# Optimization experiments

Hardware: AMD Instinct MI355X
Metric: run time of the kernel (lower is better)

Reference implementation:

```python
import jax, jax.numpy as jnp
import numpy as np

G, M_PER_GROUP, K, N = 8, 2048, 4096, 4096  # experts, tokens/expert, d_model, expert out dim


def setup_inputs() -> dict:
    key = jax.random.key(0)
    k1, k2, k3, k4 = jax.random.split(key, 4)
    T = G * M_PER_GROUP
    # int8 quantized activations [total_tokens, K] and per-expert weights [G, N, K] ('NT' layout)
    i8_left_tensor = jax.random.randint(k1, (T, K), -127, 128, dtype=jnp.int32).astype(jnp.int8)
    i8_right_tensors = jax.random.randint(k2, (G, N, K), -127, 128, dtype=jnp.int32).astype(jnp.int8)
    # per-token and per-(group, out-channel) dequant scales
    left_scales = jax.random.uniform(k3, (T,), jnp.float32, 0.001, 0.02)
    right_scales = jax.random.uniform(k4, (G, N), jnp.float32, 0.001, 0.02)
    tokens_per_group = jnp.full((G,), M_PER_GROUP, dtype=jnp.int32)
    return {
        "i8_left_tensor": i8_left_tensor,
        "i8_right_tensors": i8_right_tensors,
        "left_scales": left_scales,
        "right_scales": right_scales,
        "tokens_per_group": tokens_per_group,
    }


def reference(i8_left_tensor, i8_right_tensors, left_scales, right_scales, tokens_per_group):
    # moe_w8a8_group_gemm, 'NT': per group g, out_g = (A_g @ B_g^T) * ls_g[:, None] * rs_g[None, :] -> fp16
    g, n, k = i8_right_tensors.shape
    t = i8_left_tensor.shape[0]
    m = t // g  # equal-sized groups (tokens_per_group is constant M_PER_GROUP)
    a = i8_left_tensor.reshape(g, m, k).astype(jnp.float32)   # [G, M, K]
    b = i8_right_tensors.astype(jnp.float32)                  # [G, N, K]
    acc = jnp.einsum('gmk,gnk->gmn', a, b)                    # int8xint8 accum in f32
    ls = left_scales.reshape(g, m, 1)
    rs = right_scales[:, None, :]
    out = (acc * ls * rs).astype(jnp.float16)                 # fused dequant epilogue
    return out.reshape(t, n)
```

## Files before the change

kernel.cpp:

```cpp
#include <hip/hip_runtime.h>

#define GG 8
#define MPG 2048
#define KD 4096
#define ND 4096

using i32x4 = __attribute__((ext_vector_type(4))) int;

__device__ __forceinline__ int pack4(i32x4 v) {
  return (int)((unsigned)(v[0] & 0xff) | ((unsigned)(v[1] & 0xff) << 8) |
               ((unsigned)(v[2] & 0xff) << 16) | ((unsigned)(v[3] & 0xff) << 24));
}

__global__ void conv_kernel(const int* __restrict__ src, char* __restrict__ dst, long nelem) {
  long t = (long)blockIdx.x * blockDim.x + threadIdx.x;
  long stride = (long)gridDim.x * blockDim.x;
  for (long e = t * 16; e < nelem; e += stride * 16) {
    i32x4 x0 = *(const i32x4*)(src + e);
    i32x4 x1 = *(const i32x4*)(src + e + 4);
    i32x4 x2 = *(const i32x4*)(src + e + 8);
    i32x4 x3 = *(const i32x4*)(src + e + 12);
    i32x4 p;
    p[0] = pack4(x0); p[1] = pack4(x1); p[2] = pack4(x2); p[3] = pack4(x3);
    *(i32x4*)(dst + e) = p;
  }
}

__device__ __forceinline__ void gload_lds16(const void* g, void* l) {
  __builtin_amdgcn_global_load_lds(
      (const __attribute__((address_space(1))) unsigned int*)g,
      (__attribute__((address_space(3))) unsigned int*)l, 16, 0, 0);
}

#define CFENCE() asm volatile("" ::: "memory")

constexpr int NT = KD / 128;

__global__ __launch_bounds__(256, 2) void gemm256x128_i8(
    const char* __restrict__ Aall,
    const char* __restrict__ Ball,
    const float* __restrict__ ls,
    const float* __restrict__ rs,
    float* __restrict__ out,
    int g0, int nwg)
{
  extern __shared__ char lds[];

  const int tid  = threadIdx.x;
  const int lane = tid & 63;
  const int wave = tid >> 6;

  int bid = blockIdx.x;
  int wg  = (bid & 7) * (nwg >> 3) + (bid >> 3);
  const int gl = wg >> 8;
  const int rr_ = wg & 255;
  const int bm = (rr_ >> 5) * 256;
  const int bn = (rr_ & 31) * 128;
  const int g  = g0 + gl;

  const int srow = tid >> 3;
  const int scol = ((tid & 7) << 4) ^ ((srow & 7) << 4);
  const char* Ag = Aall + ((size_t)gl * MPG + bm) * KD;
  const char* Bg = Ball + ((size_t)gl * ND  + bn) * KD;
  const int voff = srow * KD + scol;
  char* wbase = lds + wave * 1024;

  auto stage = [&](int kt) {
    const int ko = kt << 7;
#pragma unroll
    for (int i = 0; i < 8; ++i)
      gload_lds16(Ag + (size_t)(ko + voff) + (size_t)i * (32 * KD), wbase + i * 4096);
#pragma unroll
    for (int i = 0; i < 4; ++i)
      gload_lds16(Bg + (size_t)(ko + voff) + (size_t)i * (32 * KD), wbase + 32768 + i * 4096);
  };

  const int wm = wave >> 1;
  const int wn = wave & 1;
  const int r16 = lane & 15;
  const int klane = (lane >> 4) << 4;
  const int sx = (r16 & 7) << 4;
  const char* pA = lds + (size_t)(wm * 128 + r16) * 128;
  const char* pB = lds + 32768 + (size_t)(wn * 64 + r16) * 128;
  const int kx0 = klane ^ sx;
  const int kx1 = (64 + klane) ^ sx;

  i32x4 acc[8][4] = {};

  stage(0);
  asm volatile("s_waitcnt vmcnt(0)" ::: "memory");
  __builtin_amdgcn_s_barrier();
  CFENCE();

#pragma unroll 1
  for (int kt = 0; kt < NT; ++kt) {
    i32x4 bf0[4], bf1[4], af0[4], af1[4];
#pragma unroll
    for (int n = 0; n < 4; ++n) bf0[n] = *(const i32x4*)(pB + n * 2048 + kx0);
#pragma unroll
    for (int m = 0; m < 4; ++m) af0[m] = *(const i32x4*)(pA + m * 2048 + kx0);
#pragma unroll
    for (int m = 0; m < 4; ++m) af1[m] = *(const i32x4*)(pA + (4 + m) * 2048 + kx0);
    __builtin_amdgcn_s_setprio(1);
#pragma unroll
    for (int m = 0; m < 4; ++m)
#pragma unroll
      for (int n = 0; n < 4; ++n)
        acc[m][n] = __builtin_amdgcn_mfma_i32_16x16x64_i8(af0[m], bf0[n], acc[m][n], 0, 0, 0);
    __builtin_amdgcn_s_setprio(0);
#pragma unroll
    for (int n = 0; n < 4; ++n) bf1[n] = *(const i32x4*)(pB + n * 2048 + kx1);
#pragma unroll
    for (int m = 0; m < 4; ++m) af0[m] = *(const i32x4*)(pA + m * 2048 + kx1);
    __builtin_amdgcn_s_setprio(1);
#pragma unroll
    for (int m = 0; m < 4; ++m)
#pragma unroll
      for (int n = 0; n < 4; ++n)
        acc[4 + m][n] = __builtin_amdgcn_mfma_i32_16x16x64_i8(af1[m], bf0[n], acc[4 + m][n], 0, 0, 0);
    __builtin_amdgcn_s_setprio(0);
#pragma unroll
    for (int m = 0; m < 4; ++m) af1[m] = *(const i32x4*)(pA + (4 + m) * 2048 + kx1);
    __builtin_amdgcn_s_setprio(1);
#pragma unroll
    for (int m = 0; m < 4; ++m)
#pragma unroll
      for (int n = 0; n < 4; ++n)
        acc[m][n] = __builtin_amdgcn_mfma_i32_16x16x64_i8(af0[m], bf1[n], acc[m][n], 0, 0, 0);
#pragma unroll
    for (int m = 0; m < 4; ++m)
#pragma unroll
      for (int n = 0; n < 4; ++n)
        acc[4 + m][n] = __builtin_amdgcn_mfma_i32_16x16x64_i8(af1[m], bf1[n], acc[4 + m][n], 0, 0, 0);
    __builtin_amdgcn_s_setprio(0);

    asm volatile("s_waitcnt lgkmcnt(0)" ::: "memory");
    __builtin_amdgcn_sched_barrier(0);
    __builtin_amdgcn_s_barrier();
    CFENCE();
    if (kt + 1 < NT) stage(kt + 1);
    asm volatile("s_waitcnt vmcnt(0)" ::: "memory");
    __builtin_amdgcn_s_barrier();
    CFENCE();
  }

  const size_t orow0 = (size_t)g * MPG + bm + wm * 128 + ((lane >> 4) << 2);
  const int col0 = bn + wn * 64 + r16;
  float rsv[4];
#pragma unroll
  for (int n = 0; n < 4; ++n) rsv[n] = rs[(size_t)g * ND + col0 + n * 16];
#pragma unroll
  for (int m = 0; m < 8; ++m) {
#pragma unroll
    for (int q = 0; q < 4; ++q) {
      size_t row = orow0 + m * 16 + q;
      float lsv = ls[row];
#pragma unroll
      for (int n = 0; n < 4; ++n)
        out[row * ND + col0 + n * 16] = (float)acc[m][n][q] * lsv * rsv[n];
    }
  }
}

constexpr int BM = 128, BN = 128, BK = 64;

template<bool DIRECT>
__global__ __launch_bounds__(256) void gemm_i8(
    const void* __restrict__ Aptr, const void* __restrict__ Bptr,
    const float* __restrict__ ls, const float* __restrict__ rs,
    float* __restrict__ out, int g0)
{
  __shared__ char lA[BM * BK];
  __shared__ char lB[BN * BK];

  const int gl = blockIdx.z;
  const int g = g0 + gl;
  const int bm = blockIdx.y * BM;
  const int bn = blockIdx.x * BN;
  const int tid = threadIdx.x;
  const int lane = tid & 63;
  const int wave = tid >> 6;
  const int wr = (wave >> 1) * 64;
  const int wc = (wave & 1) * 64;
  const int r16 = lane & 15;
  const int kb = (lane >> 4) * 16;

  i32x4 acc[4][4] = {};

  if constexpr (!DIRECT) {
    const char* Ag = (const char*)Aptr + ((size_t)gl * MPG + bm) * KD;
    const char* Bg = (const char*)Bptr + ((size_t)gl * ND + bn) * KD;
    const int srow = tid >> 2;
    const int skoff = (tid & 3) * 16;
    const char* pa0 = Ag + (size_t)srow * KD + skoff;
    const char* pa1 = Ag + (size_t)(srow + 64) * KD + skoff;
    const char* pb0 = Bg + (size_t)srow * KD + skoff;
    const char* pb1 = Bg + (size_t)(srow + 64) * KD + skoff;
    char* la0 = lA + wave * 1024;
    char* la1 = lA + 4096 + wave * 1024;
    char* lb0 = lB + wave * 1024;
    char* lb1 = lB + 4096 + wave * 1024;

    for (int k0 = 0; k0 < KD; k0 += BK) {
      gload_lds16(pa0 + k0, la0);
      gload_lds16(pa1 + k0, la1);
      gload_lds16(pb0 + k0, lb0);
      gload_lds16(pb1 + k0, lb1);
      __syncthreads();
      i32x4 af[4], bf[4];
#pragma unroll
      for (int m = 0; m < 4; ++m) af[m] = *(const i32x4*)(lA + (wr + m * 16 + r16) * BK + kb);
#pragma unroll
      for (int n = 0; n < 4; ++n) bf[n] = *(const i32x4*)(lB + (wc + n * 16 + r16) * BK + kb);
#pragma unroll
      for (int m = 0; m < 4; ++m)
#pragma unroll
        for (int n = 0; n < 4; ++n)
          acc[m][n] = __builtin_amdgcn_mfma_i32_16x16x64_i8(af[m], bf[n], acc[m][n], 0, 0, 0);
      __syncthreads();
    }
  } else {
    const int* Ag = (const int*)Aptr + ((size_t)gl * MPG + bm) * KD;
    const int* Bg = (const int*)Bptr + ((size_t)gl * ND + bn) * KD;
    const int drow = tid >> 1;
    const int dk = (tid & 1) * 32;

    for (int k0 = 0; k0 < KD; k0 += BK) {
      int pa[8], pb[8];
#pragma unroll
      for (int j = 0; j < 8; ++j) pa[j] = pack4(*(const i32x4*)(Ag + (size_t)drow * KD + k0 + dk + j * 4));
#pragma unroll
      for (int j = 0; j < 8; ++j) pb[j] = pack4(*(const i32x4*)(Bg + (size_t)drow * KD + k0 + dk + j * 4));
      __syncthreads();
      *(i32x4*)(lA + drow * 64 + dk)      = *(i32x4*)(pa);
      *(i32x4*)(lA + drow * 64 + dk + 16) = *(i32x4*)(pa + 4);
      *(i32x4*)(lB + drow * 64 + dk)      = *(i32x4*)(pb);
      *(i32x4*)(lB + drow * 64 + dk + 16) = *(i32x4*)(pb + 4);
      __syncthreads();
      i32x4 af[4], bf[4];
#pragma unroll
      for (int m = 0; m < 4; ++m) af[m] = *(const i32x4*)(lA + (wr + m * 16 + r16) * BK + kb);
#pragma unroll
      for (int n = 0; n < 4; ++n) bf[n] = *(const i32x4*)(lB + (wc + n * 16 + r16) * BK + kb);
#pragma unroll
      for (int m = 0; m < 4; ++m)
#pragma unroll
        for (int n = 0; n < 4; ++n)
          acc[m][n] = __builtin_amdgcn_mfma_i32_16x16x64_i8(af[m], bf[n], acc[m][n], 0, 0, 0);
    }
  }

  const size_t trow0 = (size_t)g * MPG + bm + wr + (lane >> 4) * 4;
  const int col0 = bn + wc + r16;
  float rsv[4];
#pragma unroll
  for (int n = 0; n < 4; ++n) rsv[n] = rs[(size_t)g * ND + col0 + n * 16];
#pragma unroll
  for (int m = 0; m < 4; ++m) {
#pragma unroll
    for (int q = 0; q < 4; ++q) {
      size_t row = trow0 + m * 16 + q;
      float lsv = ls[row];
#pragma unroll
      for (int n = 0; n < 4; ++n)
        out[row * ND + col0 + n * 16] = (float)acc[m][n][q] * lsv * rsv[n];
    }
  }
}

extern "C" void kernel_launch(void* const* d_in, const int* in_sizes, int n_in,
                              void* d_out, int out_size, void* d_ws, size_t ws_size,
                              hipStream_t stream) {
  const int* A32 = (const int*)d_in[0];
  const int* B32 = (const int*)d_in[1];
  const float* ls = (const float*)d_in[2];
  const float* rs = (const float*)d_in[3];
  float* out = (float*)d_out;

  const size_t aE = (size_t)GG * MPG * KD;
  const size_t bE = (size_t)GG * ND * KD;
  const size_t aSlab = (size_t)MPG * KD;
  const size_t bSlab = (size_t)ND * KD;

  const int smem = 49152;
  bool big_lds_ok =
      hipFuncSetAttribute((const void*)gemm256x128_i8,
                          hipFuncAttributeMaxDynamicSharedMemorySize, smem) == hipSuccess;

  if (d_ws && ws_size >= aE + bE) {
    char* wsA = (char*)d_ws;
    char* wsB = wsA + aE;
    conv_kernel<<<8192, 256, 0, stream>>>(A32, wsA, (long)aE);
    conv_kernel<<<16384, 256, 0, stream>>>(B32, wsB, (long)bE);
    if (big_lds_ok) {
      gemm256x128_i8<<<2048, 256, smem, stream>>>(wsA, wsB, ls, rs, out, 0, 2048);
    } else {
      dim3 grid(ND / BN, MPG / BM, GG);
      gemm_i8<false><<<grid, dim3(256), 0, stream>>>(wsA, wsB, ls, rs, out, 0);
    }
  } else if (d_ws && ws_size >= aSlab + bSlab) {
    char* wsA = (char*)d_ws;
    char* wsB = wsA + aSlab;
    for (int gidx = 0; gidx < GG; ++gidx) {
      conv_kernel<<<2048, 256, 0, stream>>>(A32 + (size_t)gidx * aSlab, wsA, (long)aSlab);
      conv_kernel<<<4096, 256, 0, stream>>>(B32 + (size_t)gidx * bSlab, wsB, (long)bSlab);
      if (big_lds_ok) {
        gemm256x128_i8<<<256, 256, smem, stream>>>(wsA, wsB, ls, rs, out, gidx, 256);
      } else {
        dim3 grid(ND / BN, MPG / BM, 1);
        gemm_i8<false><<<grid, dim3(256), 0, stream>>>(wsA, wsB, ls, rs, out, gidx);
      }
    }
  } else {
    dim3 grid(ND / BN, MPG / BM, GG);
    gemm_i8<true><<<grid, dim3(256), 0, stream>>>(A32, B32, ls, rs, out, 0);
  }
}
```

Before: 508.6 us.

## Overlap next group's int32-to-int8 conversion with current group's GEMM

The inputs arrive as int32 and must be packed to int8 before the GEMM. Previously all groups were converted up front in two large kernels, followed by one big GEMM launch. Now only group 0 is converted up front, and each group's GEMM launch carries 256 extra blocks that convert the next group's slab. This hides conversion bandwidth behind MFMA compute, at the cost of eight launches instead of one and only 256 GEMM blocks per launch, which may underfill the GPU and lose cross-group tail overlap.

Measured after the change: 591.5 us. 1.16x slower.

```diff
diff --git a/kernel.cpp b/kernel.cpp
--- a/kernel.cpp
+++ b/kernel.cpp
@@ -12,18 +12,20 @@
                ((unsigned)(v[2] & 0xff) << 16) | ((unsigned)(v[3] & 0xff) << 24));
 }
 
+__device__ __forceinline__ void pack16(const int* __restrict__ src, char* __restrict__ dst, long e) {
+  i32x4 x0 = *(const i32x4*)(src + e);
+  i32x4 x1 = *(const i32x4*)(src + e + 4);
+  i32x4 x2 = *(const i32x4*)(src + e + 8);
+  i32x4 x3 = *(const i32x4*)(src + e + 12);
+  i32x4 p;
+  p[0] = pack4(x0); p[1] = pack4(x1); p[2] = pack4(x2); p[3] = pack4(x3);
+  *(i32x4*)(dst + e) = p;
+}
+
 __global__ void conv_kernel(const int* __restrict__ src, char* __restrict__ dst, long nelem) {
   long t = (long)blockIdx.x * blockDim.x + threadIdx.x;
-  long stride = (long)gridDim.x * blockDim.x;
-  for (long e = t * 16; e < nelem; e += stride * 16) {
-    i32x4 x0 = *(const i32x4*)(src + e);
-    i32x4 x1 = *(const i32x4*)(src + e + 4);
-    i32x4 x2 = *(const i32x4*)(src + e + 8);
-    i32x4 x3 = *(const i32x4*)(src + e + 12);
-    i32x4 p;
-    p[0] = pack4(x0); p[1] = pack4(x1); p[2] = pack4(x2); p[3] = pack4(x3);
-    *(i32x4*)(dst + e) = p;
-  }
+  long stride = (long)gridDim.x * blockDim.x * 16;
+  for (long e = t * 16; e < nelem; e += stride) pack16(src, dst, e);
 }
 
 __device__ __forceinline__ void gload_lds16(const void* g, void* l) {
@@ -34,34 +36,53 @@
 
 #define CFENCE() asm volatile("" ::: "memory")
 
-constexpr int NT = KD / 128;
-
-__global__ __launch_bounds__(256, 2) void gemm256x128_i8(
-    const char* __restrict__ Aall,
-    const char* __restrict__ Ball,
+constexpr int NTK = KD / 128;
+constexpr int NCONV = 256;
+
+__global__ __launch_bounds__(256, 2) void fused_i8(
+    const char* __restrict__ Ag8,
+    const char* __restrict__ Bg8,
     const float* __restrict__ ls,
     const float* __restrict__ rs,
     float* __restrict__ out,
-    int g0, int nwg)
+    int g,
+    const int* __restrict__ A32,
+    const int* __restrict__ B32,
+    char* __restrict__ wsA,
+    char* __restrict__ wsB,
+    int gnext)
 {
   extern __shared__ char lds[];
-
-  const int tid  = threadIdx.x;
+  const int tid = threadIdx.x;
+
+  if (blockIdx.x >= 256) {
+    if (gnext < GG) {
+      const long aSlab = (long)MPG * KD;
+      const long bSlab = (long)ND * KD;
+      const long t = (long)(blockIdx.x - 256) * 256 + tid;
+      const long stride = (long)NCONV * 256 * 16;
+      const int* srcA = A32 + (size_t)gnext * aSlab;
+      char* dstA = wsA + (size_t)gnext * aSlab;
+      for (long e = t * 16; e < aSlab; e += stride) pack16(srcA, dstA, e);
+      const int* srcB = B32 + (size_t)gnext * bSlab;
+      char* dstB = wsB + (size_t)gnext * bSlab;
+      for (long e = t * 16; e < bSlab; e += stride) pack16(srcB, dstB, e);
+    }
+    return;
+  }
+
   const int lane = tid & 63;
   const int wave = tid >> 6;
 
-  int bid = blockIdx.x;
-  int wg  = (bid & 7) * (nwg >> 3) + (bid >> 3);
-  const int gl = wg >> 8;
-  const int rr_ = wg & 255;
-  const int bm = (rr_ >> 5) * 256;
-  const int bn = (rr_ & 31) * 128;
-  const int g  = g0 + gl;
+  const int bid = blockIdx.x;
+  const int wg = (bid & 7) * 32 + (bid >> 3);
+  const int bm = (wg >> 5) * 256;
+  const int bn = (wg & 31) * 128;
 
   const int srow = tid >> 3;
   const int scol = ((tid & 7) << 4) ^ ((srow & 7) << 4);
-  const char* Ag = Aall + ((size_t)gl * MPG + bm) * KD;
-  const char* Bg = Ball + ((size_t)gl * ND  + bn) * KD;
+  const char* Ag = Ag8 + (size_t)bm * KD;
+  const char* Bg = Bg8 + (size_t)bn * KD;
   const int voff = srow * KD + scol;
   char* wbase = lds + wave * 1024;
 
@@ -93,7 +114,7 @@
   CFENCE();
 
 #pragma unroll 1
-  for (int kt = 0; kt < NT; ++kt) {
+  for (int kt = 0; kt < NTK; ++kt) {
     i32x4 bf0[4], bf1[4], af0[4], af1[4];
 #pragma unroll
     for (int n = 0; n < 4; ++n) bf0[n] = *(const i32x4*)(pB + n * 2048 + kx0);
@@ -138,7 +159,7 @@
     __builtin_amdgcn_sched_barrier(0);
     __builtin_amdgcn_s_barrier();
     CFENCE();
-    if (kt + 1 < NT) stage(kt + 1);
+    if (kt + 1 < NTK) stage(kt + 1);
     asm volatile("s_waitcnt vmcnt(0)" ::: "memory");
     __builtin_amdgcn_s_barrier();
     CFENCE();
@@ -284,32 +305,35 @@
 
   const int smem = 49152;
   bool big_lds_ok =
-      hipFuncSetAttribute((const void*)gemm256x128_i8,
+      hipFuncSetAttribute((const void*)fused_i8,
                           hipFuncAttributeMaxDynamicSharedMemorySize, smem) == hipSuccess;
 
-  if (d_ws && ws_size >= aE + bE) {
+  if (d_ws && ws_size >= aE + bE && big_lds_ok) {
+    char* wsA = (char*)d_ws;
+    char* wsB = wsA + aE;
+    conv_kernel<<<1024, 256, 0, stream>>>(A32, wsA, (long)aSlab);
+    conv_kernel<<<2048, 256, 0, stream>>>(B32, wsB, (long)bSlab);
+    for (int g = 0; g < GG; ++g) {
+      fused_i8<<<256 + NCONV, 256, smem, stream>>>(
+          wsA + (size_t)g * aSlab, wsB + (size_t)g * bSlab,
+          ls, rs, out, g,
+          A32, B32, wsA, wsB, g + 1);
+    }
+  } else if (d_ws && ws_size >= aE + bE) {
     char* wsA = (char*)d_ws;
     char* wsB = wsA + aE;
     conv_kernel<<<8192, 256, 0, stream>>>(A32, wsA, (long)aE);
     conv_kernel<<<16384, 256, 0, stream>>>(B32, wsB, (long)bE);
-    if (big_lds_ok) {
-      gemm256x128_i8<<<2048, 256, smem, stream>>>(wsA, wsB, ls, rs, out, 0, 2048);
-    } else {
-      dim3 grid(ND / BN, MPG / BM, GG);
-      gemm_i8<false><<<grid, dim3(256), 0, stream>>>(wsA, wsB, ls, rs, out, 0);
-    }
+    dim3 grid(ND / BN, MPG / BM, GG);
+    gemm_i8<false><<<grid, dim3(256), 0, stream>>>(wsA, wsB, ls, rs, out, 0);
   } else if (d_ws && ws_size >= aSlab + bSlab) {
     char* wsA = (char*)d_ws;
     char* wsB = wsA + aSlab;
     for (int gidx = 0; gidx < GG; ++gidx) {
       conv_kernel<<<2048, 256, 0, stream>>>(A32 + (size_t)gidx * aSlab, wsA, (long)aSlab);
       conv_kernel<<<4096, 256, 0, stream>>>(B32 + (size_t)gidx * bSlab, wsB, (long)bSlab);
-      if (big_lds_ok) {
-        gemm256x128_i8<<<256, 256, smem, stream>>>(wsA, wsB, ls, rs, out, gidx, 256);
-      } else {
-        dim3 grid(ND / BN, MPG / BM, 1);
-        gemm_i8<false><<<grid, dim3(256), 0, stream>>>(wsA, wsB, ls, rs, out, gidx);
-      }
+      dim3 grid(ND / BN, MPG / BM, 1);
+      gemm_i8<false><<<grid, dim3(256), 0, stream>>>(wsA, wsB, ls, rs, out, gidx);
     }
   } else {
     dim3 grid(ND / BN, MPG / BM, GG);
```
